# Performance work log

Measured on AMD Instinct MI355X. Metric: run time of the kernel, lower is better.

## Reference

```python
import jax, jax.numpy as jnp
import numpy as np

N, E, F, G, OUT, L = 100000, 1600000, 64, 128, 32, 2


def setup_inputs() -> dict:
    key = jax.random.key(0)
    ks = jax.random.split(key, 14)
    x = jax.random.normal(ks[0], (N, F), jnp.float32)
    src = jax.random.randint(ks[1], (E,), 0, N)
    dst = jax.random.randint(ks[2], (E,), 0, N)
    dst = dst.at[:N].set(jnp.arange(N))  # every node receives >=1 message (no empty segments)
    edge_index = jnp.stack([src, dst]).astype(jnp.int64)
    batch = jnp.sort(jnp.concatenate([jnp.arange(G), jax.random.randint(ks[3], (N - G,), 0, G)])).astype(jnp.int64)
    s = 1.0 / np.sqrt(F)
    Wlin = jax.random.normal(ks[4], (L, F, F), jnp.float32) * s   # per-layer message Linear
    blin = jnp.zeros((L, F), jnp.float32)
    t = jax.random.uniform(ks[5], (L, F), jnp.float32)            # convex bias weight in [0,1]
    Wproj = jax.random.normal(ks[6], (L, 5), jnp.float32) * 0.5   # lin_project(5->1) weight
    bproj = jnp.zeros((L,), jnp.float32)
    Wc = jax.random.normal(ks[7], (L, F, F), jnp.float32) * s     # LTSum combine Linear
    bc = jnp.zeros((L, F), jnp.float32)
    gWlin = jax.random.normal(ks[8], (F, F), jnp.float32) * s     # global conv message Linear
    gblin = jnp.zeros((F,), jnp.float32)
    gt = jax.random.uniform(ks[9], (F,), jnp.float32)
    gWproj = jax.random.normal(ks[10], (5,), jnp.float32) * 0.5
    gbproj = jnp.zeros((), jnp.float32)
    Wout = jax.random.normal(ks[11], (OUT, F), jnp.float32) * s   # out_MLP (single Linear)
    bout = jnp.zeros((OUT,), jnp.float32)
    return dict(x=x, edge_index=edge_index, batch=batch, Wlin=Wlin, blin=blin, t=t,
                Wproj=Wproj, bproj=bproj, Wc=Wc, bc=bc, gWlin=gWlin, gblin=gblin,
                gt=gt, gWproj=gWproj, gbproj=gbproj, Wout=Wout, bout=bout)


def _adaptive_relu(m, idx, num_seg, t, Wproj, bproj):
    # m: [S, F] multiset elements, idx: [S] segment ids
    mn = jax.ops.segment_min(m, idx, num_segments=num_seg)
    mx = jax.ops.segment_max(m, idx, num_segments=num_seg)
    sm = jax.ops.segment_sum(m, idx, num_segments=num_seg)
    cnt = jax.ops.segment_sum(jnp.ones((m.shape[0],), m.dtype), idx, num_segments=num_seg)
    bias = t * mx[idx] + (1.0 - t) * mn[idx]                      # gather per-segment stats
    relu_sum = jax.ops.segment_sum(jax.nn.relu(m - bias), idx, num_segments=num_seg)
    cnt_b = jnp.broadcast_to(cnt[:, None], mn.shape)
    coords = jnp.stack([cnt_b, mn, mx, relu_sum, sm], axis=-1)    # [num_seg, F, 5]
    return jnp.einsum('sfc,c->sf', coords, Wproj) + bproj


def reference(x, edge_index, batch, Wlin, blin, t, Wproj, bproj, Wc, bc,
              gWlin, gblin, gt, gWproj, gbproj, Wout, bout):
    src, dst = edge_index[0], edge_index[1]
    h = x
    for l in range(L):
        msg = h[src] @ Wlin[l].T + blin[l]                        # gather + linear message
        agg = _adaptive_relu(msg, dst, N, jnp.clip(t[l], 0.0, 1.0), Wproj[l], bproj[l])
        h = h @ Wc[l].T + bc[l] + agg                             # LTSum combine
    gmsg = h @ gWlin.T + gblin                                    # global conv message
    emb = _adaptive_relu(gmsg, batch, G, jnp.clip(gt, 0.0, 1.0), gWproj, gbproj)
    return emb @ Wout.T + bout                                    # out_MLP -> [G, OUT]
```

## Files before the change

kernel.cpp:

```cpp
#include <hip/hip_runtime.h>
#include <hip/hip_fp16.h>

#define N_NODES 100000
#define E_EDGES 1600000
#define FDIM 64
#define G_GRAPHS 128
#define OUTD 32
#define CAP 16
#define NPB 512
#define NPB_SH 9
#define KBUK ((N_NODES + NPB - 1) / NPB)
#define CAPB 10240
#define SEB 4096
#define SEBLK ((E_EDGES + SEB - 1) / SEB)
#define GCH 16

__device__ __forceinline__ __half2 u2h(unsigned int u) {
    union { unsigned int i; __half2 h; } c; c.i = u; return c.h;
}
__device__ __forceinline__ unsigned int h2u(__half2 h) {
    union { __half2 h; unsigned int i; } c; c.h = h; return c.i;
}
__device__ __forceinline__ __half2 sxh2(__half2 v, int off) {
    return u2h((unsigned int)__shfl_xor((int)h2u(v), off));
}
__device__ __forceinline__ __half2 h2min(__half2 a, __half2 b) {
    unsigned int r, x = h2u(a), y = h2u(b);
    asm("v_pk_min_f16 %0, %1, %2" : "=v"(r) : "v"(x), "v"(y));
    return u2h(r);
}
__device__ __forceinline__ __half2 h2max(__half2 a, __half2 b) {
    unsigned int r, x = h2u(a), y = h2u(b);
    asm("v_pk_max_f16 %0, %1, %2" : "=v"(r) : "v"(x), "v"(y));
    return u2h(r);
}
__device__ __forceinline__ __half2 h2add(__half2 a, __half2 b) {
    unsigned int r, x = h2u(a), y = h2u(b);
    asm("v_pk_add_f16 %0, %1, %2" : "=v"(r) : "v"(x), "v"(y));
    return u2h(r);
}


__global__ __launch_bounds__(256) void bound_kernel(const int* __restrict__ batch,
                                                    int* __restrict__ gstart,
                                                    int* __restrict__ bucketCursor) {
    int i = blockIdx.x * 256 + threadIdx.x;
    if (blockIdx.x == 0 && threadIdx.x < KBUK)
        bucketCursor[threadIdx.x * 16] = threadIdx.x * CAPB;
    if (i >= N_NODES) return;
    if (i == 0) {
        gstart[batch[0]] = 0;
    } else {
        int b = batch[i], pb = batch[i - 1];
        if (b != pb) gstart[b] = i;
    }
}

__global__ __launch_bounds__(256) void bscatter_kernel(const int* __restrict__ src,
                                                       const int* __restrict__ dst,
                                                       int* __restrict__ bucketCursor,
                                                       int* __restrict__ ebuf) {
    __shared__ int h[KBUK], resbase[KBUK], lcur[KBUK];
    for (int i = threadIdx.x; i < KBUK; i += 256) { h[i] = 0; lcur[i] = 0; }
    __syncthreads();
    const int base = blockIdx.x * SEB;
#pragma unroll
    for (int i = 0; i < 16; ++i) {
        int e = base + i * 256 + threadIdx.x;
        if (e < E_EDGES) atomicAdd(&h[dst[e] >> NPB_SH], 1);
    }
    __syncthreads();
    for (int i = threadIdx.x; i < KBUK; i += 256)
        resbase[i] = h[i] ? atomicAdd(&bucketCursor[i * 16], h[i]) : 0;
    __syncthreads();
#pragma unroll
    for (int i = 0; i < 16; ++i) {
        int e = base + i * 256 + threadIdx.x;
        if (e < E_EDGES) {
            int d = dst[e];
            int b = d >> NPB_SH;
            int pos = resbase[b] + atomicAdd(&lcur[b], 1);
            ebuf[pos] = (src[e] << NPB_SH) | (d & (NPB - 1));
        }
    }
}

__global__ __launch_bounds__(256) void bscan_kernel(const int* __restrict__ bucketCursor,
                                                    int* __restrict__ bucketStart,
                                                    int* __restrict__ offsets) {
    __shared__ int s[256];
    const int tid = threadIdx.x;
    int v = (tid < KBUK) ? (bucketCursor[tid * 16] - tid * CAPB) : 0;
    s[tid] = v;
    __syncthreads();
    for (int off = 1; off < 256; off <<= 1) {
        int t = 0;
        if (tid >= off) t = s[tid - off];
        __syncthreads();
        if (tid >= off) s[tid] += t;
        __syncthreads();
    }
    int excl = s[tid] - v;
    if (tid < KBUK) bucketStart[tid] = excl;
    if (tid == 0) { bucketStart[KBUK] = E_EDGES; offsets[N_NODES] = E_EDGES; }
}

__global__ __launch_bounds__(256) void bsort_kernel(const int* __restrict__ ebuf,
                                                    const int* __restrict__ bucketStart,
                                                    int* __restrict__ offsets,
                                                    int* __restrict__ srcSorted) {
    __shared__ int cnt[NPB];
    __shared__ int cur[NPB];
    __shared__ int wsum[4];
    const int b = blockIdx.x;
    const int tid = threadIdx.x;
    const int rbase = b * CAPB;
    const int ebase = bucketStart[b];
    const int cb = bucketStart[b + 1] - ebase;
    const int nbase = b * NPB;
    cnt[tid] = 0; cnt[tid + 256] = 0;
    __syncthreads();
    for (int e = tid; e < cb; e += 256)
        atomicAdd(&cnt[ebuf[rbase + e] & (NPB - 1)], 1);
    __syncthreads();
    int v0 = cnt[2 * tid], v1 = cnt[2 * tid + 1];
    int s = v0 + v1;
    const int lane = tid & 63, wv = tid >> 6;
    int incl = s;
#pragma unroll
    for (int off = 1; off < 64; off <<= 1) {
        int o = __shfl_up(incl, off);
        if (lane >= off) incl += o;
    }
    if (lane == 63) wsum[wv] = incl;
    __syncthreads();
    int wpre = 0;
#pragma unroll
    for (int w = 0; w < 4; ++w) wpre += (w < wv) ? wsum[w] : 0;
    int excl = wpre + incl - s;
    cur[2 * tid] = excl; cur[2 * tid + 1] = excl + v0;
    int n0 = nbase + 2 * tid;
    if (n0 < N_NODES) offsets[n0] = ebase + excl;
    if (n0 + 1 < N_NODES) offsets[n0 + 1] = ebase + excl + v0;
    __syncthreads();
    for (int e = tid; e < cb; e += 256) {
        int u = ebuf[rbase + e];
        int pos = ebase + atomicAdd(&cur[u & (NPB - 1)], 1);
        srcSorted[pos] = (u >> NPB_SH) << 4;
    }
}


template <bool DUAL>
__global__ __launch_bounds__(256) void lin_kernel(const float* __restrict__ in,
                                                  const float* __restrict__ Wm,
                                                  const float* __restrict__ bm,
                                                  const float* __restrict__ Wc,
                                                  const float* __restrict__ bc,
                                                  __half* __restrict__ outMsg,
                                                  float* __restrict__ outC) {
    extern __shared__ float4 sh[];
    const int tid = threadIdx.x;
    const int base = blockIdx.x * 64;
#pragma unroll
    for (int i = 0; i < 4; ++i) {
        int j = tid + i * 256;
        int row = j >> 4, col = j & 15;
        int swz = row * 16 + (col ^ ((row >> 2) & 7));
        if (base + row < N_NODES)
            sh[swz] = ((const float4*)in)[(size_t)base * 16 + j];
        sh[1024 + swz] = ((const float4*)Wm)[j];
        if (DUAL) sh[2048 + swz] = ((const float4*)Wc)[j];
    }
    __syncthreads();
    const int fj = tid & 15, ni = tid >> 4;
    float accM[4][4] = {{0}}, accC[4][4] = {{0}};
    const int hs = ni & 7;
    const int ws = fj & 7;
#pragma unroll 1
    for (int kk = 0; kk < 16; ++kk) {
        const int hk = kk ^ hs, wk = kk ^ ws;
        float4 h0 = sh[(4 * ni + 0) * 16 + hk];
        float4 h1 = sh[(4 * ni + 1) * 16 + hk];
        float4 h2 = sh[(4 * ni + 2) * 16 + hk];
        float4 h3 = sh[(4 * ni + 3) * 16 + hk];
#pragma unroll
        for (int j = 0; j < 4; ++j) {
            float4 wv = sh[1024 + (4 * fj + j) * 16 + wk];
            accM[0][j] += h0.x * wv.x + h0.y * wv.y + h0.z * wv.z + h0.w * wv.w;
            accM[1][j] += h1.x * wv.x + h1.y * wv.y + h1.z * wv.z + h1.w * wv.w;
            accM[2][j] += h2.x * wv.x + h2.y * wv.y + h2.z * wv.z + h2.w * wv.w;
            accM[3][j] += h3.x * wv.x + h3.y * wv.y + h3.z * wv.z + h3.w * wv.w;
            if (DUAL) {
                float4 cv = sh[2048 + (4 * fj + j) * 16 + wk];
                accC[0][j] += h0.x * cv.x + h0.y * cv.y + h0.z * cv.z + h0.w * cv.w;
                accC[1][j] += h1.x * cv.x + h1.y * cv.y + h1.z * cv.z + h1.w * cv.w;
                accC[2][j] += h2.x * cv.x + h2.y * cv.y + h2.z * cv.z + h2.w * cv.w;
                accC[3][j] += h3.x * cv.x + h3.y * cv.y + h3.z * cv.z + h3.w * cv.w;
            }
        }
    }
    float4 bm4 = *(const float4*)(bm + 4 * fj);
    float4 bc4 = DUAL ? *(const float4*)(bc + 4 * fj) : make_float4(0, 0, 0, 0);
#pragma unroll
    for (int r = 0; r < 4; ++r) {
        int node = base + 4 * ni + r;
        if (node < N_NODES) {
            uint2 st;
            st.x = h2u(__floats2half2_rn(accM[r][0] + bm4.x, accM[r][1] + bm4.y));
            st.y = h2u(__floats2half2_rn(accM[r][2] + bm4.z, accM[r][3] + bm4.w));
            *(uint2*)(outMsg + (size_t)node * 64 + 4 * fj) = st;
            if (DUAL) {
                float4 c = make_float4(accC[r][0] + bc4.x, accC[r][1] + bc4.y,
                                       accC[r][2] + bc4.z, accC[r][3] + bc4.w);
                *(float4*)(outC + (size_t)node * 64 + 4 * fj) = c;
            }
        }
    }
}


__global__ __launch_bounds__(256) void agg_kernel(const __half* __restrict__ msgH,
                                                  const int* __restrict__ offsets,
                                                  const int* __restrict__ srcSorted,
                                                  const float* __restrict__ tptr,
                                                  const float* __restrict__ Wp,
                                                  const float* __restrict__ bp,
                                                  float* __restrict__ hbuf) {
    __shared__ uint2 cache[4][CAP][16];
    const int w = threadIdx.x >> 6;
    const int lane = threadIdx.x & 63;
    const int g = lane >> 4;
    const int fq = lane & 15;
    const int node = blockIdx.x * 4 + w;
    if (node >= N_NODES) return;
    const int start = offsets[node], end = offsets[node + 1];
    const int deg = end - start;
    const uint2* mq = (const uint2*)msgH + fq;
    const float INF = 65504.f;
    __half2 mnA = __float2half2_rn(INF),  mnB = __float2half2_rn(INF);
    __half2 mxA = __float2half2_rn(-INF), mxB = __float2half2_rn(-INF);
    __half2 smA = __float2half2_rn(0.f),  smB = __float2half2_rn(0.f);

#define ACCU(u) { __half2 a_ = u2h((u).x), b_ = u2h((u).y); \
    mnA = h2min(mnA, a_); mxA = h2max(mxA, a_); smA = h2add(smA, a_); \
    mnB = h2min(mnB, b_); mxB = h2max(mxB, b_); smB = h2add(smB, b_); }

    if (deg >= 16) {
        {
            int i0 = start + g;
            int s0 = srcSorted[i0], s1 = srcSorted[i0 + 4];
            int s2 = srcSorted[i0 + 8], s3 = srcSorted[i0 + 12];
            uint2 u0 = mq[(size_t)s0], u1 = mq[(size_t)s1];
            uint2 u2 = mq[(size_t)s2], u3 = mq[(size_t)s3];
            cache[w][g][fq] = u0; cache[w][g + 4][fq] = u1;
            cache[w][g + 8][fq] = u2; cache[w][g + 12][fq] = u3;
            ACCU(u0) ACCU(u1) ACCU(u2) ACCU(u3)
        }
        int e = start + 16;
        for (; e + 16 <= end; e += 16) {
            int i0 = e + g;
            int s0 = srcSorted[i0], s1 = srcSorted[i0 + 4];
            int s2 = srcSorted[i0 + 8], s3 = srcSorted[i0 + 12];
            uint2 u0 = mq[(size_t)s0], u1 = mq[(size_t)s1];
            uint2 u2 = mq[(size_t)s2], u3 = mq[(size_t)s3];
            ACCU(u0) ACCU(u1) ACCU(u2) ACCU(u3)
        }
        if (e < end) {
            int i0 = e + g, i1 = i0 + 4, i2 = i0 + 8, i3 = i0 + 12;
            bool ok0 = i0 < end, ok1 = i1 < end, ok2 = i2 < end, ok3 = i3 < end;
            int s0 = 0, s1 = 0, s2 = 0, s3 = 0;
            if (ok0) s0 = srcSorted[i0];
            if (ok1) s1 = srcSorted[i1];
            if (ok2) s2 = srcSorted[i2];
            if (ok3) s3 = srcSorted[i3];
            uint2 u0, u1, u2, u3;
            if (ok0) u0 = mq[(size_t)s0];
            if (ok1) u1 = mq[(size_t)s1];
            if (ok2) u2 = mq[(size_t)s2];
            if (ok3) u3 = mq[(size_t)s3];
            if (ok0) ACCU(u0)
            if (ok1) ACCU(u1)
            if (ok2) ACCU(u2)
            if (ok3) ACCU(u3)
        }
    } else {
        int i0 = start + g, i1 = i0 + 4, i2 = i0 + 8, i3 = i0 + 12;
        bool ok0 = i0 < end, ok1 = i1 < end, ok2 = i2 < end, ok3 = i3 < end;
        int s0 = 0, s1 = 0, s2 = 0, s3 = 0;
        if (ok0) s0 = srcSorted[i0];
        if (ok1) s1 = srcSorted[i1];
        if (ok2) s2 = srcSorted[i2];
        if (ok3) s3 = srcSorted[i3];
        uint2 u0, u1, u2, u3;
        if (ok0) u0 = mq[(size_t)s0];
        if (ok1) u1 = mq[(size_t)s1];
        if (ok2) u2 = mq[(size_t)s2];
        if (ok3) u3 = mq[(size_t)s3];
        if (ok0) { cache[w][g][fq] = u0;      ACCU(u0) }
        if (ok1) { cache[w][g + 4][fq] = u1;  ACCU(u1) }
        if (ok2) { cache[w][g + 8][fq] = u2;  ACCU(u2) }
        if (ok3) { cache[w][g + 12][fq] = u3; ACCU(u3) }
    }
#pragma unroll
    for (int off = 16; off <= 32; off <<= 1) {
        mnA = h2min(mnA, sxh2(mnA, off)); mnB = h2min(mnB, sxh2(mnB, off));
        mxA = h2max(mxA, sxh2(mxA, off)); mxB = h2max(mxB, sxh2(mxB, off));
        smA = h2add(smA, sxh2(smA, off)); smB = h2add(smB, sxh2(smB, off));
    }
    float mn0 = __low2float(mnA), mn1 = __high2float(mnA);
    float mn2 = __low2float(mnB), mn3 = __high2float(mnB);
    float mx0 = __low2float(mxA), mx1 = __high2float(mxA);
    float mx2 = __low2float(mxB), mx3 = __high2float(mxB);
    float4 tv = *(const float4*)(tptr + 4 * fq);
    tv.x = fminf(fmaxf(tv.x, 0.f), 1.f); tv.y = fminf(fmaxf(tv.y, 0.f), 1.f);
    tv.z = fminf(fmaxf(tv.z, 0.f), 1.f); tv.w = fminf(fmaxf(tv.w, 0.f), 1.f);
    float b0 = tv.x * mx0 + (1.f - tv.x) * mn0;
    float b1 = tv.y * mx1 + (1.f - tv.y) * mn1;
    float b2 = tv.z * mx2 + (1.f - tv.z) * mn2;
    float b3 = tv.w * mx3 + (1.f - tv.w) * mn3;
    __half2 biasA = __floats2half2_rn(b0, b1);
    __half2 biasB = __floats2half2_rn(b2, b3);
    float fb0 = __low2float(biasA), fb1 = __high2float(biasA);
    float fb2 = __low2float(biasB), fb3 = __high2float(biasB);
    __half2 rsA = __float2half2_rn(0.f), rsB = __float2half2_rn(0.f);

#define RACCU(u) { __half2 a_ = u2h((u).x), b_ = u2h((u).y); \
    rsA = h2add(rsA, h2max(a_, biasA)); \
    rsB = h2add(rsB, h2max(b_, biasB)); }

    if (deg >= 16) {
#pragma unroll
        for (int i = 0; i < 4; ++i) {
            uint2 u = cache[w][i * 4 + g][fq];
            RACCU(u)
        }
        int e = start + 16;
        for (; e + 16 <= end; e += 16) {
            int i0 = e + g;
            int s0 = srcSorted[i0], s1 = srcSorted[i0 + 4];
            int s2 = srcSorted[i0 + 8], s3 = srcSorted[i0 + 12];
            uint2 u0 = mq[(size_t)s0], u1 = mq[(size_t)s1];
            uint2 u2 = mq[(size_t)s2], u3 = mq[(size_t)s3];
            RACCU(u0) RACCU(u1) RACCU(u2) RACCU(u3)
        }
        if (e < end) {
            int i0 = e + g, i1 = i0 + 4, i2 = i0 + 8, i3 = i0 + 12;
            bool ok0 = i0 < end, ok1 = i1 < end, ok2 = i2 < end, ok3 = i3 < end;
            int s0 = 0, s1 = 0, s2 = 0, s3 = 0;
            if (ok0) s0 = srcSorted[i0];
            if (ok1) s1 = srcSorted[i1];
            if (ok2) s2 = srcSorted[i2];
            if (ok3) s3 = srcSorted[i3];
            uint2 u0, u1, u2, u3;
            if (ok0) u0 = mq[(size_t)s0];
            if (ok1) u1 = mq[(size_t)s1];
            if (ok2) u2 = mq[(size_t)s2];
            if (ok3) u3 = mq[(size_t)s3];
            if (ok0) RACCU(u0)
            if (ok1) RACCU(u1)
            if (ok2) RACCU(u2)
            if (ok3) RACCU(u3)
        }
    } else {
        for (int idx = start + g; idx < end; idx += 4) {
            uint2 u = cache[w][idx - start][fq];
            RACCU(u)
        }
    }
#pragma unroll
    for (int off = 16; off <= 32; off <<= 1) {
        rsA = h2add(rsA, sxh2(rsA, off));
        rsB = h2add(rsB, sxh2(rsB, off));
    }
    if (g == 0) {
        float cnt = (float)deg;
        float w0 = Wp[0], w1 = Wp[1], w2 = Wp[2], w3 = Wp[3], w4 = Wp[4], bp0 = bp[0];
        float rs0 = __low2float(rsA) - cnt * fb0;
        float rs1 = __high2float(rsA) - cnt * fb1;
        float rs2 = __low2float(rsB) - cnt * fb2;
        float rs3 = __high2float(rsB) - cnt * fb3;
        float sm0 = __low2float(smA), sm1 = __high2float(smA);
        float sm2 = __low2float(smB), sm3 = __high2float(smB);
        float4* hp = (float4*)(hbuf + (size_t)node * 64 + 4 * fq);
        float4 h = *hp;
        h.x += w0 * cnt + w1 * mn0 + w2 * mx0 + w3 * rs0 + w4 * sm0 + bp0;
        h.y += w0 * cnt + w1 * mn1 + w2 * mx1 + w3 * rs1 + w4 * sm1 + bp0;
        h.z += w0 * cnt + w1 * mn2 + w2 * mx2 + w3 * rs2 + w4 * sm2 + bp0;
        h.w += w0 * cnt + w1 * mn3 + w2 * mx3 + w3 * rs3 + w4 * sm3 + bp0;
        *hp = h;
    }
#undef ACCU
#undef RACCU
}


__global__ __launch_bounds__(256) void gaggA_kernel(const __half* __restrict__ msgH,
                                                    const int* __restrict__ gstart,
                                                    float* __restrict__ pmn,
                                                    float* __restrict__ pmx,
                                                    float* __restrict__ psm) {
    const int bid = blockIdx.x;
    const int g = bid >> 4, c = bid & (GCH - 1);
    const int s = gstart[g];
    const int e = (g == G_GRAPHS - 1) ? N_NODES : gstart[g + 1];
    const int clen = (e - s + GCH - 1) / GCH;
    const int cs = s + c * clen;
    const int ce = (cs + clen < e) ? (cs + clen) : e;
    const int f = threadIdx.x & 63, r = threadIdx.x >> 6;
    float mn = __builtin_inff(), mx = -__builtin_inff(), sm = 0.f;
    for (int i = cs + r; i < ce; i += 4) {
        float v = __half2float(msgH[(size_t)i * 64 + f]);
        mn = fminf(mn, v); mx = fmaxf(mx, v); sm += v;
    }
    __shared__ float smn[4][64], smx[4][64], ssm[4][64];
    smn[r][f] = mn; smx[r][f] = mx; ssm[r][f] = sm;
    __syncthreads();
    if (r == 0) {
        pmn[bid * 64 + f] = fminf(fminf(smn[0][f], smn[1][f]), fminf(smn[2][f], smn[3][f]));
        pmx[bid * 64 + f] = fmaxf(fmaxf(smx[0][f], smx[1][f]), fmaxf(smx[2][f], smx[3][f]));
        psm[bid * 64 + f] = ssm[0][f] + ssm[1][f] + ssm[2][f] + ssm[3][f];
    }
}

__global__ __launch_bounds__(64) void gaggB_kernel(const float* __restrict__ pmn,
                                                   const float* __restrict__ pmx,
                                                   const float* __restrict__ psm,
                                                   const float* __restrict__ gt,
                                                   float* __restrict__ gMn,
                                                   float* __restrict__ gMx,
                                                   float* __restrict__ gSm,
                                                   float* __restrict__ gBias) {
    const int g = blockIdx.x, f = threadIdx.x;
    float mn = __builtin_inff(), mx = -__builtin_inff(), sm = 0.f;
#pragma unroll
    for (int c = 0; c < GCH; ++c) {
        int i = (g * GCH + c) * 64 + f;
        mn = fminf(mn, pmn[i]); mx = fmaxf(mx, pmx[i]); sm += psm[i];
    }
    float tv = fminf(fmaxf(gt[f], 0.f), 1.f);
    gMn[g * 64 + f] = mn; gMx[g * 64 + f] = mx; gSm[g * 64 + f] = sm;
    gBias[g * 64 + f] = tv * mx + (1.f - tv) * mn;
}

__global__ __launch_bounds__(256) void gaggC_kernel(const __half* __restrict__ msgH,
                                                    const int* __restrict__ gstart,
                                                    const float* __restrict__ gBias,
                                                    float* __restrict__ prs) {
    const int bid = blockIdx.x;
    const int g = bid >> 4, c = bid & (GCH - 1);
    const int s = gstart[g];
    const int e = (g == G_GRAPHS - 1) ? N_NODES : gstart[g + 1];
    const int clen = (e - s + GCH - 1) / GCH;
    const int cs = s + c * clen;
    const int ce = (cs + clen < e) ? (cs + clen) : e;
    const int f = threadIdx.x & 63, r = threadIdx.x >> 6;
    const float bias = gBias[g * 64 + f];
    float rs = 0.f;
    for (int i = cs + r; i < ce; i += 4) {
        float v = __half2float(msgH[(size_t)i * 64 + f]);
        rs += fmaxf(v - bias, 0.f);
    }
    __shared__ float srs[4][64];
    srs[r][f] = rs;
    __syncthreads();
    if (r == 0)
        prs[bid * 64 + f] = srs[0][f] + srs[1][f] + srs[2][f] + srs[3][f];
}

__global__ __launch_bounds__(64) void gaggD_kernel(const float* __restrict__ prs,
                                                   const int* __restrict__ gstart,
                                                   const float* __restrict__ gMn,
                                                   const float* __restrict__ gMx,
                                                   const float* __restrict__ gSm,
                                                   const float* __restrict__ gWp,
                                                   const float* __restrict__ gbp,
                                                   const float* __restrict__ Wout,
                                                   const float* __restrict__ bout,
                                                   float* __restrict__ out) {
    const int g = blockIdx.x, f = threadIdx.x;
    float rs = 0.f;
#pragma unroll
    for (int c = 0; c < GCH; ++c) rs += prs[(g * GCH + c) * 64 + f];
    const int s = gstart[g];
    const int e = (g == G_GRAPHS - 1) ? N_NODES : gstart[g + 1];
    float cnt = (float)(e - s);
    __shared__ float emb[64];
    emb[f] = gWp[0] * cnt + gWp[1] * gMn[g * 64 + f] + gWp[2] * gMx[g * 64 + f] +
             gWp[3] * rs + gWp[4] * gSm[g * 64 + f] + gbp[0];
    __syncthreads();
    if (f < OUTD) {
        float a = bout[f];
        const float* wr = Wout + f * 64;
#pragma unroll
        for (int k = 0; k < 64; ++k) a = fmaf(emb[k], wr[k], a);
        out[g * OUTD + f] = a;
    }
}


extern "C" void kernel_launch(void* const* d_in, const int* in_sizes, int n_in,
                              void* d_out, int out_size, void* d_ws, size_t ws_size,
                              hipStream_t stream) {
    const float* x     = (const float*)d_in[0];
    const int*   ei    = (const int*)d_in[1];
    const int*   batch = (const int*)d_in[2];
    const float* Wlin  = (const float*)d_in[3];
    const float* blin  = (const float*)d_in[4];
    const float* t     = (const float*)d_in[5];
    const float* Wproj = (const float*)d_in[6];
    const float* bproj = (const float*)d_in[7];
    const float* Wc    = (const float*)d_in[8];
    const float* bc    = (const float*)d_in[9];
    const float* gWlin = (const float*)d_in[10];
    const float* gblin = (const float*)d_in[11];
    const float* gt    = (const float*)d_in[12];
    const float* gWproj= (const float*)d_in[13];
    const float* gbproj= (const float*)d_in[14];
    const float* Wout  = (const float*)d_in[15];
    const float* bout  = (const float*)d_in[16];
    float* out = (float*)d_out;

    const int* src = ei;
    const int* dst = ei + E_EDGES;

    char* p = (char*)d_ws;
    float* bufH   = (float*)p; p += (size_t)N_NODES * FDIM * sizeof(float);
    __half* msgH  = (__half*)p; p += (size_t)N_NODES * FDIM * sizeof(__half);
    int* ebuf     = (int*)p;   p += (size_t)KBUK * CAPB * sizeof(int);
    int* offsets  = (int*)p;   p += (size_t)(N_NODES + 1) * sizeof(int);
    int* gstart   = (int*)p;   p += (size_t)G_GRAPHS * sizeof(int);
    int* bucketStart  = (int*)p; p += (size_t)(KBUK + 1) * sizeof(int);
    int* bucketCursor = (int*)p; p += (size_t)KBUK * 16 * sizeof(int);
    int* srcSorted= (int*)p;   p += (size_t)E_EDGES * sizeof(int);
    float* pmn = (float*)p;    p += (size_t)G_GRAPHS * GCH * 64 * sizeof(float);
    float* pmx = (float*)p;    p += (size_t)G_GRAPHS * GCH * 64 * sizeof(float);
    float* psm = (float*)p;    p += (size_t)G_GRAPHS * GCH * 64 * sizeof(float);
    float* prs = (float*)p;    p += (size_t)G_GRAPHS * GCH * 64 * sizeof(float);
    float* gMn = (float*)p;    p += (size_t)G_GRAPHS * 64 * sizeof(float);
    float* gMx = (float*)p;    p += (size_t)G_GRAPHS * 64 * sizeof(float);
    float* gSm = (float*)p;    p += (size_t)G_GRAPHS * 64 * sizeof(float);
    float* gBias = (float*)p;  p += (size_t)G_GRAPHS * 64 * sizeof(float);

    const int NB = (N_NODES + 255) / 256;
    bound_kernel<<<NB, 256, 0, stream>>>(batch, gstart, bucketCursor);
    bscatter_kernel<<<SEBLK, 256, 0, stream>>>(src, dst, bucketCursor, ebuf);
    bscan_kernel<<<1, 256, 0, stream>>>(bucketCursor, bucketStart, offsets);
    bsort_kernel<<<KBUK, 256, 0, stream>>>(ebuf, bucketStart, offsets, srcSorted);

    const int LB = (N_NODES + 63) / 64;
    const int AB = (N_NODES + 3) / 4;
    const size_t LDS_DUAL = 3 * 1024 * sizeof(float4);
    const size_t LDS_SINGLE = 2 * 1024 * sizeof(float4);

    lin_kernel<true><<<LB, 256, LDS_DUAL, stream>>>(x, Wlin, blin, Wc, bc, msgH, bufH);
    agg_kernel<<<AB, 256, 0, stream>>>(msgH, offsets, srcSorted, t, Wproj, bproj, bufH);
    lin_kernel<true><<<LB, 256, LDS_DUAL, stream>>>(bufH, Wlin + 4096, blin + 64,
                                                    Wc + 4096, bc + 64, msgH, bufH);
    agg_kernel<<<AB, 256, 0, stream>>>(msgH, offsets, srcSorted, t + 64, Wproj + 5,
                                       bproj + 1, bufH);
    lin_kernel<false><<<LB, 256, LDS_SINGLE, stream>>>(bufH, gWlin, gblin, nullptr,
                                                       nullptr, msgH, nullptr);
    gaggA_kernel<<<G_GRAPHS * GCH, 256, 0, stream>>>(msgH, gstart, pmn, pmx, psm);
    gaggB_kernel<<<G_GRAPHS, 64, 0, stream>>>(pmn, pmx, psm, gt, gMn, gMx, gSm, gBias);
    gaggC_kernel<<<G_GRAPHS * GCH, 256, 0, stream>>>(msgH, gstart, gBias, prs);
    gaggD_kernel<<<G_GRAPHS, 64, 0, stream>>>(prs, gstart, gMn, gMx, gSm, gWproj,
                                              gbproj, Wout, bout, out);
}
```

Before: 278.0 us.

## Cache up to 32 gathered messages in LDS and store linear weights as fp16

```diff
diff --git a/kernel.cpp b/kernel.cpp
--- a/kernel.cpp
+++ b/kernel.cpp
@@ -6,7 +6,7 @@
 #define FDIM 64
 #define G_GRAPHS 128
 #define OUTD 32
-#define CAP 16
+#define CAP 32
 #define NPB 512
 #define NPB_SH 9
 #define KBUK ((N_NODES + NPB - 1) / NPB)
@@ -160,6 +160,8 @@
                                                   __half* __restrict__ outMsg,
                                                   float* __restrict__ outC) {
     extern __shared__ float4 sh[];
+    uint2* shWm = (uint2*)&sh[1024];
+    uint2* shWc = shWm + 1024;
     const int tid = threadIdx.x;
     const int base = blockIdx.x * 64;
 #pragma unroll
@@ -169,8 +171,18 @@
         int swz = row * 16 + (col ^ ((row >> 2) & 7));
         if (base + row < N_NODES)
             sh[swz] = ((const float4*)in)[(size_t)base * 16 + j];
-        sh[1024 + swz] = ((const float4*)Wm)[j];
-        if (DUAL) sh[2048 + swz] = ((const float4*)Wc)[j];
+        float4 wm = ((const float4*)Wm)[j];
+        uint2 pm;
+        pm.x = h2u(__floats2half2_rn(wm.x, wm.y));
+        pm.y = h2u(__floats2half2_rn(wm.z, wm.w));
+        shWm[swz] = pm;
+        if (DUAL) {
+            float4 wc = ((const float4*)Wc)[j];
+            uint2 pc;
+            pc.x = h2u(__floats2half2_rn(wc.x, wc.y));
+            pc.y = h2u(__floats2half2_rn(wc.z, wc.w));
+            shWc[swz] = pc;
+        }
     }
     __syncthreads();
     const int fj = tid & 15, ni = tid >> 4;
@@ -186,17 +198,23 @@
         float4 h3 = sh[(4 * ni + 3) * 16 + hk];
 #pragma unroll
         for (int j = 0; j < 4; ++j) {
-            float4 wv = sh[1024 + (4 * fj + j) * 16 + wk];
-            accM[0][j] += h0.x * wv.x + h0.y * wv.y + h0.z * wv.z + h0.w * wv.w;
-            accM[1][j] += h1.x * wv.x + h1.y * wv.y + h1.z * wv.z + h1.w * wv.w;
-            accM[2][j] += h2.x * wv.x + h2.y * wv.y + h2.z * wv.z + h2.w * wv.w;
-            accM[3][j] += h3.x * wv.x + h3.y * wv.y + h3.z * wv.z + h3.w * wv.w;
+            uint2 wu = shWm[(4 * fj + j) * 16 + wk];
+            __half2 wl = u2h(wu.x), wh = u2h(wu.y);
+            float m0 = __low2float(wl), m1 = __high2float(wl);
+            float m2 = __low2float(wh), m3 = __high2float(wh);
+            accM[0][j] += h0.x * m0 + h0.y * m1 + h0.z * m2 + h0.w * m3;
+            accM[1][j] += h1.x * m0 + h1.y * m1 + h1.z * m2 + h1.w * m3;
+            accM[2][j] += h2.x * m0 + h2.y * m1 + h2.z * m2 + h2.w * m3;
+            accM[3][j] += h3.x * m0 + h3.y * m1 + h3.z * m2 + h3.w * m3;
             if (DUAL) {
-                float4 cv = sh[2048 + (4 * fj + j) * 16 + wk];
-                accC[0][j] += h0.x * cv.x + h0.y * cv.y + h0.z * cv.z + h0.w * cv.w;
-                accC[1][j] += h1.x * cv.x + h1.y * cv.y + h1.z * cv.z + h1.w * cv.w;
-                accC[2][j] += h2.x * cv.x + h2.y * cv.y + h2.z * cv.z + h2.w * cv.w;
-                accC[3][j] += h3.x * cv.x + h3.y * cv.y + h3.z * cv.z + h3.w * cv.w;
+                uint2 cu = shWc[(4 * fj + j) * 16 + wk];
+                __half2 cl = u2h(cu.x), ch = u2h(cu.y);
+                float c0 = __low2float(cl), c1 = __high2float(cl);
+                float c2 = __low2float(ch), c3 = __high2float(ch);
+                accC[0][j] += h0.x * c0 + h0.y * c1 + h0.z * c2 + h0.w * c3;
+                accC[1][j] += h1.x * c0 + h1.y * c1 + h1.z * c2 + h1.w * c3;
+                accC[2][j] += h2.x * c0 + h2.y * c1 + h2.z * c2 + h2.w * c3;
+                accC[3][j] += h3.x * c0 + h3.y * c1 + h3.z * c2 + h3.w * c3;
             }
         }
     }
@@ -264,6 +282,11 @@
             int s2 = srcSorted[i0 + 8], s3 = srcSorted[i0 + 12];
             uint2 u0 = mq[(size_t)s0], u1 = mq[(size_t)s1];
             uint2 u2 = mq[(size_t)s2], u3 = mq[(size_t)s3];
+            int sb = e - start;
+            if (sb < CAP) {
+                cache[w][sb + g][fq] = u0;      cache[w][sb + g + 4][fq] = u1;
+                cache[w][sb + g + 8][fq] = u2;  cache[w][sb + g + 12][fq] = u3;
+            }
             ACCU(u0) ACCU(u1) ACCU(u2) ACCU(u3)
         }
         if (e < end) {
@@ -279,10 +302,11 @@
             if (ok1) u1 = mq[(size_t)s1];
             if (ok2) u2 = mq[(size_t)s2];
             if (ok3) u3 = mq[(size_t)s3];
-            if (ok0) ACCU(u0)
-            if (ok1) ACCU(u1)
-            if (ok2) ACCU(u2)
-            if (ok3) ACCU(u3)
+            int sb = e - start;
+            if (ok0) { if (sb + g < CAP)      cache[w][sb + g][fq] = u0;      ACCU(u0) }
+            if (ok1) { if (sb + g + 4 < CAP)  cache[w][sb + g + 4][fq] = u1;  ACCU(u1) }
+            if (ok2) { if (sb + g + 8 < CAP)  cache[w][sb + g + 8][fq] = u2;  ACCU(u2) }
+            if (ok3) { if (sb + g + 12 < CAP) cache[w][sb + g + 12][fq] = u3; ACCU(u3) }
         }
     } else {
         int i0 = start + g, i1 = i0 + 4, i2 = i0 + 8, i3 = i0 + 12;
@@ -335,16 +359,12 @@
             uint2 u = cache[w][i * 4 + g][fq];
             RACCU(u)
         }
-        int e = start + 16;
-        for (; e + 16 <= end; e += 16) {
-            int i0 = e + g;
-            int s0 = srcSorted[i0], s1 = srcSorted[i0 + 4];
-            int s2 = srcSorted[i0 + 8], s3 = srcSorted[i0 + 12];
-            uint2 u0 = mq[(size_t)s0], u1 = mq[(size_t)s1];
-            uint2 u2 = mq[(size_t)s2], u3 = mq[(size_t)s3];
-            RACCU(u0) RACCU(u1) RACCU(u2) RACCU(u3)
-        }
-        if (e < end) {
+        const int cend = (end < start + CAP) ? end : (start + CAP);
+        for (int idx = start + 16 + g; idx < cend; idx += 4) {
+            uint2 u = cache[w][idx - start][fq];
+            RACCU(u)
+        }
+        for (int e = start + CAP; e < end; e += 16) {
             int i0 = e + g, i1 = i0 + 4, i2 = i0 + 8, i3 = i0 + 12;
             bool ok0 = i0 < end, ok1 = i1 < end, ok2 = i2 < end, ok3 = i3 < end;
             int s0 = 0, s1 = 0, s2 = 0, s3 = 0;
@@ -550,8 +570,8 @@
 
     const int LB = (N_NODES + 63) / 64;
     const int AB = (N_NODES + 3) / 4;
-    const size_t LDS_DUAL = 3 * 1024 * sizeof(float4);
-    const size_t LDS_SINGLE = 2 * 1024 * sizeof(float4);
+    const size_t LDS_DUAL = 16384 + 8192 + 8192;
+    const size_t LDS_SINGLE = 16384 + 8192;
 
     lin_kernel<true><<<LB, 256, LDS_DUAL, stream>>>(x, Wlin, blin, Wc, bc, msgH, bufH);
     agg_kernel<<<AB, 256, 0, stream>>>(msgH, offsets, srcSorted, t, Wproj, bproj, bufH);
```

Result: faster. 269.3 us (-3.1%).
